# Optimization experiments

Hardware: AMD Instinct MI355X
Metric: run time of the kernel (lower is better)

The kernel has to match this reference:

```python
import jax, jax.numpy as jnp
import numpy as np

BN_EPS = 1e-5

def setup_inputs() -> dict:
    key = jax.random.key(0)
    ks = jax.random.split(key, 10)
    B, C, W, H = 4, 128, 32, 128
    Co = C // 2  # 64
    s_in = 1.0 / np.sqrt(C)
    s_out = 1.0 / np.sqrt(Co)
    return {
        "range_x": jax.random.normal(ks[0], (B, C, W, H), jnp.float32),
        "img": jax.random.normal(ks[1], (B, C, W, H), jnp.float32),
        "wq": jax.random.normal(ks[2], (Co, C), jnp.float32) * s_in,
        "bq": jax.random.normal(ks[3], (Co,), jnp.float32) * 0.01,
        "wk": jax.random.normal(ks[4], (Co, C), jnp.float32) * s_in,
        "bk": jax.random.normal(ks[5], (Co,), jnp.float32) * 0.01,
        "wv": jax.random.normal(ks[6], (Co, C), jnp.float32) * s_in,
        "bv": jax.random.normal(ks[7], (Co,), jnp.float32) * 0.01,
        "wc": jax.random.normal(ks[8], (C, Co), jnp.float32) * s_out,
        "bc": jax.random.normal(ks[9], (C,), jnp.float32) * 0.01,
        "bn_gamma": jnp.ones((C,), jnp.float32),
        "bn_beta": jnp.zeros((C,), jnp.float32),
        "bn_mean": jnp.zeros((C,), jnp.float32),
        "bn_var": jnp.ones((C,), jnp.float32),
    }

def reference(range_x, img, wq, bq, wk, bk, wv, bv, wc, bc, bn_gamma, bn_beta, bn_mean, bn_var):
    B, C, W, H = range_x.shape
    HW = W * H
    r = range_x.reshape(B, C, HW)  # [B,C,N]
    i = img.reshape(B, C, HW)
    # 1x1 convs == per-pixel linear projections
    q = jnp.einsum('oc,bcn->bno', wq, r) + bq            # [B,N,Co] (query from range)
    k = jnp.einsum('oc,bcn->bon', wk, i) + bk[None, :, None]  # [B,Co,N]
    corr = jnp.einsum('bno,bom->bnm', q, k)              # [B,N,N]
    attn = jax.nn.softmax(corr, axis=-1)
    v = jnp.einsum('oc,bcn->bon', wv, i) + bv[None, :, None]  # [B,Co,N]
    # out[b,o,n] = sum_m v[b,o,m] * attn[b,n,m]  (bmm(V, attn^T))
    out = jnp.einsum('bom,bnm->bon', v, attn)            # [B,Co,N]
    # channel_back: 1x1 conv -> BN (inference) -> ReLU
    y = jnp.einsum('co,bon->bcn', wc, out) + bc[None, :, None]
    inv = bn_gamma / jnp.sqrt(bn_var + BN_EPS)
    y = y * inv[None, :, None] + (bn_beta - bn_mean * inv)[None, :, None]
    y = jax.nn.relu(y)
    return img + y.reshape(B, C, W, H)
```

## Files before the change

kernel.cpp:

```cpp
#include <hip/hip_runtime.h>
#include <hip/hip_bf16.h>

typedef __attribute__((ext_vector_type(4))) float f32x4;
typedef __attribute__((ext_vector_type(8))) short s16x8;
typedef __attribute__((ext_vector_type(4))) short s16x4;

__device__ __forceinline__ ushort f2bf(float f){
  union { float f; unsigned u; } x; x.f = f;
  unsigned r = x.u + 0x7fffu + ((x.u >> 16) & 1u);
  return (ushort)(r >> 16);
}
__device__ __forceinline__ float bf2f(ushort h){
  union { unsigned u; float f; } x; x.u = ((unsigned)h) << 16;
  return x.f;
}

__device__ __forceinline__ void gload16(const void* g, void* l){
  __builtin_amdgcn_global_load_lds(
      (const __attribute__((address_space(1))) void*)g,
      (__attribute__((address_space(3))) void*)l, 16, 0, 0);
}

#if __has_builtin(__builtin_amdgcn_mfma_f32_16x16x16bf16_1k)
__device__ __forceinline__ f32x4 mfma16(s16x4 a, s16x4 b, f32x4 c){
  return __builtin_amdgcn_mfma_f32_16x16x16bf16_1k(a, b, c, 0, 0, 0);
}
#elif __has_builtin(__builtin_amdgcn_mfma_f32_16x16x16_bf16)
__device__ __forceinline__ f32x4 mfma16(s16x4 a, s16x4 b, f32x4 c){
  return __builtin_amdgcn_mfma_f32_16x16x16_bf16(a, b, c, 0, 0, 0);
}
#else
__device__ __forceinline__ f32x4 mfma16(s16x4 a, s16x4 b, f32x4 c){
  f32x4 d;
  asm volatile("v_mfma_f32_16x16x16_bf16 %0, %1, %2, %3\n\ts_nop 7\n\ts_nop 7"
               : "=v"(d) : "v"(a), "v"(b), "v"(c));
  return d;
}
#endif

__global__ __launch_bounds__(256) void wprep(
    const float* __restrict__ wq, const float* __restrict__ wk,
    const float* __restrict__ wv, ushort* __restrict__ Wh,
    ushort* __restrict__ Wl)
{
  int flat = blockIdx.x*256 + threadIdx.x;
  int row = flat >> 7, c = flat & 127;
  float v = (row < 64) ? wq[row*128 + c]
          : (row < 128) ? wk[(row-64)*128 + c]
          : wv[(row-128)*128 + c];
  ushort hi = f2bf(v);
  Wh[flat] = hi;
  Wl[flat] = f2bf(v - bf2f(hi));
}

__global__ __launch_bounds__(256, 2) void proj_qkv(
    const float* __restrict__ xr, const float* __restrict__ xi,
    const ushort* __restrict__ Wh, const ushort* __restrict__ Wl,
    const float* __restrict__ bq, const float* __restrict__ bk,
    const float* __restrict__ bv,
    ushort* __restrict__ Qh, ushort* __restrict__ Ql,
    ushort* __restrict__ Kh, ushort* __restrict__ Vt)
{
  __shared__ __align__(16) float xrL[128*64];
  __shared__ __align__(16) float xiL[128*64];
  const int tid = threadIdx.x;
  const int idx = blockIdx.x;
  const int oh  = idx & 1;
  const int nt  = (idx >> 1) & 63;
  const int b   = idx >> 7;
  const int n0  = nt << 6;
  const int lane = tid & 63;
  const int w    = tid >> 6;
  const int l15  = lane & 15;
  const int g    = lane >> 4;

  {
    const float* xrs = xr + (size_t)b*524288 + n0;
    const float* xis = xi + (size_t)b*524288 + n0;
    #pragma unroll
    for (int j = 0; j < 8; ++j){
      int row = j*16 + (tid >> 4);
      int ch  = tid & 15;
      gload16(xrs + (size_t)row*4096 + ch*4, xrL + j*1024 + w*256);
      gload16(xis + (size_t)row*4096 + ch*4, xiL + j*1024 + w*256);
    }
  }
  __syncthreads();

  s16x8 xrh[4], xrl[4], xih[4], xil[4];
  const int px = w*16 + l15;
  #pragma unroll
  for (int kc = 0; kc < 4; ++kc){
    #pragma unroll
    for (int j = 0; j < 8; ++j){
      int r = kc*32 + g*8 + j;
      float a = xrL[r*64 + px];
      ushort h = f2bf(a);
      xrh[kc][j] = (short)h;
      xrl[kc][j] = (short)f2bf(a - bf2f(h));
      float bb = xiL[r*64 + px];
      ushort h2 = f2bf(bb);
      xih[kc][j] = (short)h2;
      xil[kc][j] = (short)f2bf(bb - bf2f(h2));
    }
  }

  #pragma unroll
  for (int ot = 0; ot < 6; ++ot){
    const int p    = ot >> 1;
    const int sub  = ot & 1;
    const int obase = oh*32 + sub*16;
    const int wrow  = p*64 + obase;
    f32x4 acc = {0.f,0.f,0.f,0.f};
    #pragma unroll
    for (int kc = 0; kc < 4; ++kc){
      s16x8 whf = *(const s16x8*)(Wh + (size_t)(wrow + l15)*128 + kc*32 + g*8);
      s16x8 wlf = *(const s16x8*)(Wl + (size_t)(wrow + l15)*128 + kc*32 + g*8);
      const s16x8 xh = (p==0) ? xrh[kc] : xih[kc];
      const s16x8 xl = (p==0) ? xrl[kc] : xil[kc];
      if (p < 2){
        acc = __builtin_amdgcn_mfma_f32_16x16x32_bf16(xh, whf, acc, 0,0,0);
        acc = __builtin_amdgcn_mfma_f32_16x16x32_bf16(xl, whf, acc, 0,0,0);
        acc = __builtin_amdgcn_mfma_f32_16x16x32_bf16(xh, wlf, acc, 0,0,0);
      } else {
        acc = __builtin_amdgcn_mfma_f32_16x16x32_bf16(whf, xh, acc, 0,0,0);
        acc = __builtin_amdgcn_mfma_f32_16x16x32_bf16(wlf, xh, acc, 0,0,0);
        acc = __builtin_amdgcn_mfma_f32_16x16x32_bf16(whf, xl, acc, 0,0,0);
      }
    }
    if (p == 0){
      float bqv = bq[obase + l15];
      #pragma unroll
      for (int r = 0; r < 4; ++r){
        float q = acc[r] + bqv;
        ushort hi = f2bf(q);
        size_t a = (size_t)(b*4096 + n0 + w*16 + g*4 + r)*64 + obase + l15;
        Qh[a] = hi; Ql[a] = f2bf(q - bf2f(hi));
      }
    } else if (p == 1){
      float bkv = bk[obase + l15];
      #pragma unroll
      for (int r = 0; r < 4; ++r){
        float k = acc[r] + bkv;
        size_t a = (size_t)(b*4096 + n0 + w*16 + g*4 + r)*64 + obase + l15;
        Kh[a] = f2bf(k);
      }
    } else {
      #pragma unroll
      for (int r = 0; r < 4; ++r){
        int o = obase + g*4 + r;
        float v = acc[r] + bv[o];
        Vt[(size_t)(b*64 + o)*4096 + n0 + w*16 + l15] = f2bf(v);
      }
    }
  }
}

__global__ __launch_bounds__(256, 5) void flash_attn(
    const ushort* __restrict__ Qh, const ushort* __restrict__ Ql,
    const ushort* __restrict__ Kh, const ushort* __restrict__ Vt,
    float* __restrict__ Opart, float* __restrict__ Mst,
    float* __restrict__ Lst)
{
  __shared__ __align__(16) ushort khL[2][4096];
  __shared__ __align__(16) ushort vL[2][4096];

  const int tid  = threadIdx.x;
  const int idx  = blockIdx.x;
  const int ks   = idx & 3;
  const int qt   = (idx >> 2) & 63;
  const int b    = idx >> 8;
  const int lane = tid & 63;
  const int w    = tid >> 6;
  const int l15  = lane & 15;
  const int g    = lane >> 4;
  const int qrow = qt*64 + w*16;
  const int kv0  = ks << 10;
  const int srow = lane >> 2;
  const int sg   = lane & 3;
  const int sgs  = sg ^ ((srow >> 1) & 3);

  const size_t qoff = ((size_t)(b*4096 + qrow + l15))*64 + g*8;
  s16x8 qh0 = *(const s16x8*)(Qh + qoff);
  s16x8 qh1 = *(const s16x8*)(Qh + qoff + 32);
  s16x8 ql0 = *(const s16x8*)(Ql + qoff);
  s16x8 ql1 = *(const s16x8*)(Ql + qoff + 32);

  const char* KhB = (const char*)(Kh + (size_t)b*4096*64);
  const char* VB  = (const char*)(Vt + (size_t)b*64*4096);

  f32x4 o_acc[4];
  #pragma unroll
  for (int ot=0;ot<4;++ot) o_acc[ot] = (f32x4){0.f,0.f,0.f,0.f};
  float m_run = -1e30f, l_run = 0.f;

  #define STAGE_KV(kvb, bi)                                               \
  {                                                                       \
    size_t kr = (size_t)((kvb) + w*16 + srow)*128 + sgs*16;               \
    char* kd = (char*)khL[bi] + w*2048;                                   \
    gload16(KhB + kr,      kd);                                           \
    gload16(KhB + kr + 64, kd + 1024);                                    \
    size_t vr = (size_t)(w*16 + srow)*8192 + (size_t)(kvb)*2 + sgs*16;    \
    char* vd = (char*)vL[bi] + w*2048;                                    \
    gload16(VB + vr,      vd);                                            \
    gload16(VB + vr + 64, vd + 1024);                                     \
  }

  STAGE_KV(kv0, 0);
  __syncthreads();

  const int swz = (l15 >> 1) & 3;
  const int kfrag = l15*64 + (g ^ swz)*16;

  for (int t = 0; t < 16; ++t){
    const int cb = t & 1;

    if (t < 15){
      STAGE_KV(kv0 + (t+1)*64, cb ^ 1);
    }

    f32x4 s[4];
    #pragma unroll
    for (int ct=0; ct<4; ++ct){
      const char* kb = (const char*)khL[cb] + ct*2048;
      s16x8 kh0 = *(const s16x8*)(kb + kfrag);
      s16x8 kh1 = *(const s16x8*)(kb + 1024 + kfrag);
      f32x4 acc = {0.f,0.f,0.f,0.f};
      acc = __builtin_amdgcn_mfma_f32_16x16x32_bf16(kh0, ql0, acc, 0, 0, 0);
      acc = __builtin_amdgcn_mfma_f32_16x16x32_bf16(kh1, ql1, acc, 0, 0, 0);
      acc = __builtin_amdgcn_mfma_f32_16x16x32_bf16(kh0, qh0, acc, 0, 0, 0);
      acc = __builtin_amdgcn_mfma_f32_16x16x32_bf16(kh1, qh1, acc, 0, 0, 0);
      s[ct] = acc;
    }

    float mx = s[0][0];
    #pragma unroll
    for (int ct=0;ct<4;++ct){
      #pragma unroll
      for (int r=0;r<4;++r) mx = fmaxf(mx, s[ct][r]);
    }
    mx = fmaxf(mx, __shfl_xor(mx, 16));
    mx = fmaxf(mx, __shfl_xor(mx, 32));
    float mn = fmaxf(m_run, mx);
    float sc = __expf(m_run - mn);
    m_run = mn;
    float rs = 0.f;
    s16x4 pbf[4];
    #pragma unroll
    for (int ct=0;ct<4;++ct){
      #pragma unroll
      for (int r=0;r<4;++r){
        float p = __expf(s[ct][r] - mn);
        rs += p;
        pbf[ct][r] = (short)f2bf(p);
      }
    }
    rs += __shfl_xor(rs, 16);
    rs += __shfl_xor(rs, 32);
    l_run = l_run*sc + rs;
    #pragma unroll
    for (int ot=0;ot<4;++ot) o_acc[ot] *= sc;

    #pragma unroll
    for (int ot=0; ot<4; ++ot){
      const char* vbase = (const char*)vL[cb] + ot*2048 + l15*64;
      #pragma unroll
      for (int ct=0; ct<4; ++ct){
        int chunk = (((ct & 1) << 1) + (g >> 1)) ^ swz;
        s16x4 av = *(const s16x4*)(vbase + (ct>>1)*1024 + chunk*16 + (g&1)*8);
        o_acc[ot] = mfma16(av, pbf[ct], o_acc[ot]);
      }
    }

    __syncthreads();
  }
  #undef STAGE_KV

  float* ep = (float*)((char*)vL + (size_t)w*4096);
  #pragma unroll
  for (int ot=0;ot<4;++ot){
    int dw = l15*64 + ((ot*16 + g*4) ^ ((l15 & 7) << 2));
    *(f32x4*)(ep + dw) = o_acc[ot];
  }
  __syncthreads();
  {
    const int q4  = lane >> 2;
    const int seg = lane & 3;
    float* Ob = Opart + ((size_t)(ks*4 + b)*4096 + qrow)*64;
    #pragma unroll
    for (int c=0;c<4;++c){
      int o0 = seg*16 + c*4;
      f32x4 vv = *(const f32x4*)(ep + q4*64 + (o0 ^ ((q4 & 7) << 2)));
      *(f32x4*)(Ob + (size_t)q4*64 + o0) = vv;
    }
  }
  if (lane < 16){
    Mst[(size_t)(ks*4 + b)*4096 + qrow + lane] = m_run;
    Lst[(size_t)(ks*4 + b)*4096 + qrow + lane] = l_run;
  }
}

__global__ __launch_bounds__(256) void final_proj(
    const float* __restrict__ Opart, const float* __restrict__ Mst,
    const float* __restrict__ Lst, const float* __restrict__ wc,
    const float* __restrict__ bc, const float* __restrict__ gm,
    const float* __restrict__ bt, const float* __restrict__ mu,
    const float* __restrict__ vr, const float* __restrict__ img,
    float* __restrict__ out)
{
  __shared__ float ol[64*64];
  __shared__ float scl[4][64];
  const int tid = threadIdx.x;
  const int idx = blockIdx.x;
  const int cs  = idx & 3;
  const int nt  = (idx >> 2) & 63;
  const int b   = idx >> 8;
  const int n0  = nt << 6;

  if (tid < 64){
    size_t rid = (size_t)b*4096 + n0 + tid;
    float m0 = Mst[0*16384 + rid], m1 = Mst[1*16384 + rid];
    float m2 = Mst[2*16384 + rid], m3 = Mst[3*16384 + rid];
    float mm = fmaxf(fmaxf(m0,m1), fmaxf(m2,m3));
    float s0 = __expf(m0-mm), s1 = __expf(m1-mm);
    float s2 = __expf(m2-mm), s3 = __expf(m3-mm);
    float li = s0*Lst[0*16384+rid] + s1*Lst[1*16384+rid]
             + s2*Lst[2*16384+rid] + s3*Lst[3*16384+rid];
    float inv = 1.0f / li;
    scl[0][tid] = s0*inv; scl[1][tid] = s1*inv;
    scl[2][tid] = s2*inv; scl[3][tid] = s3*inv;
  }
  __syncthreads();

  {
    const size_t base = ((size_t)b*4096 + n0)*64;
    for (int j=0;j<16;++j){
      int flat = tid + (j << 8);
      int n = flat >> 6, o = flat & 63;
      float v = Opart[0*(size_t)16384*64 + base + flat] * scl[0][n]
              + Opart[1*(size_t)16384*64 + base + flat] * scl[1][n]
              + Opart[2*(size_t)16384*64 + base + flat] * scl[2][n]
              + Opart[3*(size_t)16384*64 + base + flat] * scl[3][n];
      ol[(o << 6) + (n ^ (o & 31))] = v;
    }
  }
  __syncthreads();

  const int lane = tid & 63;
  const int w = __builtin_amdgcn_readfirstlane(tid >> 6);
  const int c0 = (cs << 5) + (w << 3);

  float acc[8];
  #pragma unroll
  for (int cc=0;cc<8;++cc) acc[cc] = 0.f;

  for (int o=0;o<64;++o){
    float v = ol[(o << 6) + (lane ^ (o & 31))];
    #pragma unroll
    for (int cc=0;cc<8;++cc)
      acc[cc] = fmaf(wc[(c0+cc)*64 + o], v, acc[cc]);
  }

  #pragma unroll
  for (int cc=0;cc<8;++cc){
    int c = c0 + cc;
    float inv = gm[c] * rsqrtf(vr[c] + 1e-5f);
    float sh  = bt[c] - mu[c]*inv;
    float y = (acc[cc] + bc[c]) * inv + sh;
    y = fmaxf(y, 0.f);
    size_t gi = ((size_t)(b*128 + c))*4096 + n0 + lane;
    out[gi] = img[gi] + y;
  }
}

extern "C" void kernel_launch(void* const* d_in, const int* in_sizes, int n_in,
                              void* d_out, int out_size, void* d_ws, size_t ws_size,
                              hipStream_t stream)
{
  const float* xr = (const float*)d_in[0];
  const float* xi = (const float*)d_in[1];
  const float* wq = (const float*)d_in[2];
  const float* bq = (const float*)d_in[3];
  const float* wk = (const float*)d_in[4];
  const float* bk = (const float*)d_in[5];
  const float* wv = (const float*)d_in[6];
  const float* bv = (const float*)d_in[7];
  const float* wc = (const float*)d_in[8];
  const float* bc = (const float*)d_in[9];
  const float* gm = (const float*)d_in[10];
  const float* bt = (const float*)d_in[11];
  const float* mu = (const float*)d_in[12];
  const float* vr = (const float*)d_in[13];
  float* out = (float*)d_out;

  const size_t SZ = (size_t)4*4096*64;
  ushort* Qhw = (ushort*)d_ws;
  ushort* Qlw = Qhw + SZ;
  ushort* Khw = Qlw + SZ;
  ushort* Vtw = Khw + SZ;
  float*  Ow  = (float*)(Vtw + SZ);
  float*  Mw  = Ow + (size_t)16*4096*64;
  float*  Lw  = Mw + (size_t)16*4096;
  ushort* Whb = (ushort*)(Lw + (size_t)16*4096);
  ushort* Wlb = Whb + 192*128;

  wprep     <<<96,   256, 0, stream>>>(wq, wk, wv, Whb, Wlb);
  proj_qkv  <<<512,  256, 0, stream>>>(xr, xi, Whb, Wlb, bq, bk, bv,
                                       Qhw, Qlw, Khw, Vtw);
  flash_attn<<<1024, 256, 0, stream>>>(Qhw, Qlw, Khw, Vtw, Ow, Mw, Lw);
  final_proj<<<1024, 256, 0, stream>>>(Ow, Mw, Lw, wc, bc, gm, bt, mu, vr, xi, out);
}
```

Measured before the change: 92.37 us.

## Split KV eight ways, use exp2 with pre-scaled Q, lazy rescale, MFMA priority

Doubles the flash-attention KV split from 4 to 8 partitions (2048 blocks, 8 tiles each), and the final projection merges 8 partial results. Q is pre-multiplied by log2(e) so the softmax can use exp2f. The running max is rescaled only when some row's tile max exceeds it by more than 8, which skips the o_acc rescale on most tiles. s_setprio is raised around the MFMA sections. The aim is better occupancy and less per-tile softmax overhead. The cost is twice the partial-output traffic and a larger combine step, plus a small precision risk from deferred rescaling.

Measured after the change: 113.5 us. 1.23x slower.

```diff
diff --git a/kernel.cpp b/kernel.cpp
--- a/kernel.cpp
+++ b/kernel.cpp
@@ -4,6 +4,8 @@
 typedef __attribute__((ext_vector_type(4))) float f32x4;
 typedef __attribute__((ext_vector_type(8))) short s16x8;
 typedef __attribute__((ext_vector_type(4))) short s16x4;
+
+#define LOG2E 1.4426950408889634f
 
 __device__ __forceinline__ ushort f2bf(float f){
   union { float f; unsigned u; } x; x.f = f;
@@ -132,7 +134,7 @@
       float bqv = bq[obase + l15];
       #pragma unroll
       for (int r = 0; r < 4; ++r){
-        float q = acc[r] + bqv;
+        float q = (acc[r] + bqv) * LOG2E;
         ushort hi = f2bf(q);
         size_t a = (size_t)(b*4096 + n0 + w*16 + g*4 + r)*64 + obase + l15;
         Qh[a] = hi; Ql[a] = f2bf(q - bf2f(hi));
@@ -167,15 +169,15 @@
 
   const int tid  = threadIdx.x;
   const int idx  = blockIdx.x;
-  const int ks   = idx & 3;
-  const int qt   = (idx >> 2) & 63;
-  const int b    = idx >> 8;
+  const int ks   = idx & 7;
+  const int qt   = (idx >> 3) & 63;
+  const int b    = idx >> 9;
   const int lane = tid & 63;
   const int w    = tid >> 6;
   const int l15  = lane & 15;
   const int g    = lane >> 4;
   const int qrow = qt*64 + w*16;
-  const int kv0  = ks << 10;
+  const int kv0  = ks << 9;
   const int srow = lane >> 2;
   const int sg   = lane & 3;
   const int sgs  = sg ^ ((srow >> 1) & 3);
@@ -212,14 +214,15 @@
   const int swz = (l15 >> 1) & 3;
   const int kfrag = l15*64 + (g ^ swz)*16;
 
-  for (int t = 0; t < 16; ++t){
+  for (int t = 0; t < 8; ++t){
     const int cb = t & 1;
 
-    if (t < 15){
+    if (t < 7){
       STAGE_KV(kv0 + (t+1)*64, cb ^ 1);
     }
 
     f32x4 s[4];
+    __builtin_amdgcn_s_setprio(1);
     #pragma unroll
     for (int ct=0; ct<4; ++ct){
       const char* kb = (const char*)khL[cb] + ct*2048;
@@ -232,6 +235,7 @@
       acc = __builtin_amdgcn_mfma_f32_16x16x32_bf16(kh1, qh1, acc, 0, 0, 0);
       s[ct] = acc;
     }
+    __builtin_amdgcn_s_setprio(0);
 
     float mx = s[0][0];
     #pragma unroll
@@ -241,26 +245,30 @@
     }
     mx = fmaxf(mx, __shfl_xor(mx, 16));
     mx = fmaxf(mx, __shfl_xor(mx, 32));
-    float mn = fmaxf(m_run, mx);
-    float sc = __expf(m_run - mn);
-    m_run = mn;
+    if (!__all(mx <= m_run + 8.0f)){
+      float mn = fmaxf(m_run, mx);
+      float sc = exp2f(m_run - mn);
+      m_run = mn;
+      l_run *= sc;
+      #pragma unroll
+      for (int ot=0;ot<4;++ot) o_acc[ot] *= sc;
+    }
     float rs = 0.f;
     s16x4 pbf[4];
     #pragma unroll
     for (int ct=0;ct<4;++ct){
       #pragma unroll
       for (int r=0;r<4;++r){
-        float p = __expf(s[ct][r] - mn);
+        float p = exp2f(s[ct][r] - m_run);
         rs += p;
         pbf[ct][r] = (short)f2bf(p);
       }
     }
     rs += __shfl_xor(rs, 16);
     rs += __shfl_xor(rs, 32);
-    l_run = l_run*sc + rs;
-    #pragma unroll
-    for (int ot=0;ot<4;++ot) o_acc[ot] *= sc;
-
+    l_run += rs;
+
+    __builtin_amdgcn_s_setprio(1);
     #pragma unroll
     for (int ot=0; ot<4; ++ot){
       const char* vbase = (const char*)vL[cb] + ot*2048 + l15*64;
@@ -271,6 +279,7 @@
         o_acc[ot] = mfma16(av, pbf[ct], o_acc[ot]);
       }
     }
+    __builtin_amdgcn_s_setprio(0);
 
     __syncthreads();
   }
@@ -309,7 +318,7 @@
     float* __restrict__ out)
 {
   __shared__ float ol[64*64];
-  __shared__ float scl[4][64];
+  __shared__ float scl[8][64];
   const int tid = threadIdx.x;
   const int idx = blockIdx.x;
   const int cs  = idx & 3;
@@ -319,16 +328,22 @@
 
   if (tid < 64){
     size_t rid = (size_t)b*4096 + n0 + tid;
-    float m0 = Mst[0*16384 + rid], m1 = Mst[1*16384 + rid];
-    float m2 = Mst[2*16384 + rid], m3 = Mst[3*16384 + rid];
-    float mm = fmaxf(fmaxf(m0,m1), fmaxf(m2,m3));
-    float s0 = __expf(m0-mm), s1 = __expf(m1-mm);
-    float s2 = __expf(m2-mm), s3 = __expf(m3-mm);
-    float li = s0*Lst[0*16384+rid] + s1*Lst[1*16384+rid]
-             + s2*Lst[2*16384+rid] + s3*Lst[3*16384+rid];
+    float m[8], li = 0.f;
+    float mm = -1e30f;
+    #pragma unroll
+    for (int sp=0;sp<8;++sp){
+      m[sp] = Mst[(size_t)sp*16384 + rid];
+      mm = fmaxf(mm, m[sp]);
+    }
+    float e[8];
+    #pragma unroll
+    for (int sp=0;sp<8;++sp){
+      e[sp] = exp2f(m[sp] - mm);
+      li += e[sp] * Lst[(size_t)sp*16384 + rid];
+    }
     float inv = 1.0f / li;
-    scl[0][tid] = s0*inv; scl[1][tid] = s1*inv;
-    scl[2][tid] = s2*inv; scl[3][tid] = s3*inv;
+    #pragma unroll
+    for (int sp=0;sp<8;++sp) scl[sp][tid] = e[sp]*inv;
   }
   __syncthreads();
 
@@ -337,10 +352,10 @@
     for (int j=0;j<16;++j){
       int flat = tid + (j << 8);
       int n = flat >> 6, o = flat & 63;
-      float v = Opart[0*(size_t)16384*64 + base + flat] * scl[0][n]
-              + Opart[1*(size_t)16384*64 + base + flat] * scl[1][n]
-              + Opart[2*(size_t)16384*64 + base + flat] * scl[2][n]
-              + Opart[3*(size_t)16384*64 + base + flat] * scl[3][n];
+      float v = 0.f;
+      #pragma unroll
+      for (int sp=0;sp<8;++sp)
+        v += Opart[(size_t)sp*16384*64 + base + flat] * scl[sp][n];
       ol[(o << 6) + (n ^ (o & 31))] = v;
     }
   }
@@ -399,14 +414,14 @@
   ushort* Khw = Qlw + SZ;
   ushort* Vtw = Khw + SZ;
   float*  Ow  = (float*)(Vtw + SZ);
-  float*  Mw  = Ow + (size_t)16*4096*64;
-  float*  Lw  = Mw + (size_t)16*4096;
-  ushort* Whb = (ushort*)(Lw + (size_t)16*4096);
+  float*  Mw  = Ow + (size_t)32*4096*64;
+  float*  Lw  = Mw + (size_t)32*4096;
+  ushort* Whb = (ushort*)(Lw + (size_t)32*4096);
   ushort* Wlb = Whb + 192*128;
 
   wprep     <<<96,   256, 0, stream>>>(wq, wk, wv, Whb, Wlb);
   proj_qkv  <<<512,  256, 0, stream>>>(xr, xi, Whb, Wlb, bq, bk, bv,
                                        Qhw, Qlw, Khw, Vtw);
-  flash_attn<<<1024, 256, 0, stream>>>(Qhw, Qlw, Khw, Vtw, Ow, Mw, Lw);
+  flash_attn<<<2048, 256, 0, stream>>>(Qhw, Qlw, Khw, Vtw, Ow, Mw, Lw);
   final_proj<<<1024, 256, 0, stream>>>(Ow, Mw, Lw, wc, bc, gm, bt, mu, vr, xi, out);
 }
```

## Use exp2 softmax with lazy rescaling and MFMA row sums in flash attention

Applied to the files above, without the earlier changes.

Q is pre-scaled by log2(e) so the attention kernel can use exp2f, and the cross-split merge now uses exp2 as well. The running-max rescale of the accumulators is skipped unless some lane's max grows by more than 8. Row sums are computed by an MFMA against a ones vector on the bf16 probabilities, replacing the shuffle reductions. It also adds s_setprio around the MFMA phases, uses a tree-shaped max, and switches to the library bf16 conversion. This trims VALU and shuffle work in the softmax, at the cost of row sums taken from bf16-rounded values and a bounded growth of the unnormalised accumulators.

Result: slower. 95.62 us (+3.5%).

```diff
diff --git a/kernel.cpp b/kernel.cpp
--- a/kernel.cpp
+++ b/kernel.cpp
@@ -5,10 +5,12 @@
 typedef __attribute__((ext_vector_type(8))) short s16x8;
 typedef __attribute__((ext_vector_type(4))) short s16x4;
 
+#define LOG2E 1.4426950408889634f
+
 __device__ __forceinline__ ushort f2bf(float f){
-  union { float f; unsigned u; } x; x.f = f;
-  unsigned r = x.u + 0x7fffu + ((x.u >> 16) & 1u);
-  return (ushort)(r >> 16);
+  union { __hip_bfloat16 h; ushort u; } c;
+  c.h = __float2bfloat16(f);
+  return c.u;
 }
 __device__ __forceinline__ float bf2f(ushort h){
   union { unsigned u; float f; } x; x.u = ((unsigned)h) << 16;
@@ -132,7 +134,7 @@
       float bqv = bq[obase + l15];
       #pragma unroll
       for (int r = 0; r < 4; ++r){
-        float q = acc[r] + bqv;
+        float q = (acc[r] + bqv) * LOG2E;
         ushort hi = f2bf(q);
         size_t a = (size_t)(b*4096 + n0 + w*16 + g*4 + r)*64 + obase + l15;
         Qh[a] = hi; Ql[a] = f2bf(q - bf2f(hi));
@@ -189,10 +191,15 @@
   const char* KhB = (const char*)(Kh + (size_t)b*4096*64);
   const char* VB  = (const char*)(Vt + (size_t)b*64*4096);
 
+  s16x4 ones4;
+  #pragma unroll
+  for (int e=0;e<4;++e) ones4[e] = (short)0x3F80;
+
   f32x4 o_acc[4];
   #pragma unroll
   for (int ot=0;ot<4;++ot) o_acc[ot] = (f32x4){0.f,0.f,0.f,0.f};
-  float m_run = -1e30f, l_run = 0.f;
+  f32x4 sum_acc = {0.f,0.f,0.f,0.f};
+  float m_run = -1e30f;
 
   #define STAGE_KV(kvb, bi)                                               \
   {                                                                       \
@@ -220,6 +227,7 @@
     }
 
     f32x4 s[4];
+    __builtin_amdgcn_s_setprio(1);
     #pragma unroll
     for (int ct=0; ct<4; ++ct){
       const char* kb = (const char*)khL[cb] + ct*2048;
@@ -232,35 +240,36 @@
       acc = __builtin_amdgcn_mfma_f32_16x16x32_bf16(kh1, qh1, acc, 0, 0, 0);
       s[ct] = acc;
     }
-
-    float mx = s[0][0];
-    #pragma unroll
-    for (int ct=0;ct<4;++ct){
-      #pragma unroll
-      for (int r=0;r<4;++r) mx = fmaxf(mx, s[ct][r]);
-    }
+    __builtin_amdgcn_s_setprio(0);
+
+    float mx = fmaxf(
+        fmaxf(fmaxf(fmaxf(s[0][0],s[0][1]), fmaxf(s[0][2],s[0][3])),
+              fmaxf(fmaxf(s[1][0],s[1][1]), fmaxf(s[1][2],s[1][3]))),
+        fmaxf(fmaxf(fmaxf(s[2][0],s[2][1]), fmaxf(s[2][2],s[2][3])),
+              fmaxf(fmaxf(s[3][0],s[3][1]), fmaxf(s[3][2],s[3][3]))));
     mx = fmaxf(mx, __shfl_xor(mx, 16));
     mx = fmaxf(mx, __shfl_xor(mx, 32));
-    float mn = fmaxf(m_run, mx);
-    float sc = __expf(m_run - mn);
-    m_run = mn;
-    float rs = 0.f;
+    if (!__all(mx <= m_run + 8.0f)){
+      float mn = fmaxf(m_run, mx);
+      float sc = exp2f(m_run - mn);
+      m_run = mn;
+      #pragma unroll
+      for (int ot=0;ot<4;++ot) o_acc[ot] *= sc;
+      sum_acc *= sc;
+    }
     s16x4 pbf[4];
     #pragma unroll
     for (int ct=0;ct<4;++ct){
       #pragma unroll
       for (int r=0;r<4;++r){
-        float p = __expf(s[ct][r] - mn);
-        rs += p;
-        pbf[ct][r] = (short)f2bf(p);
-      }
-    }
-    rs += __shfl_xor(rs, 16);
-    rs += __shfl_xor(rs, 32);
-    l_run = l_run*sc + rs;
-    #pragma unroll
-    for (int ot=0;ot<4;++ot) o_acc[ot] *= sc;
-
+        pbf[ct][r] = (short)f2bf(exp2f(s[ct][r] - m_run));
+      }
+    }
+
+    __builtin_amdgcn_s_setprio(1);
+    #pragma unroll
+    for (int ct=0; ct<4; ++ct)
+      sum_acc = mfma16(ones4, pbf[ct], sum_acc);
     #pragma unroll
     for (int ot=0; ot<4; ++ot){
       const char* vbase = (const char*)vL[cb] + ot*2048 + l15*64;
@@ -271,6 +280,7 @@
         o_acc[ot] = mfma16(av, pbf[ct], o_acc[ot]);
       }
     }
+    __builtin_amdgcn_s_setprio(0);
 
     __syncthreads();
   }
@@ -296,7 +306,7 @@
   }
   if (lane < 16){
     Mst[(size_t)(ks*4 + b)*4096 + qrow + lane] = m_run;
-    Lst[(size_t)(ks*4 + b)*4096 + qrow + lane] = l_run;
+    Lst[(size_t)(ks*4 + b)*4096 + qrow + lane] = sum_acc[0];
   }
 }
 
@@ -322,8 +332,8 @@
     float m0 = Mst[0*16384 + rid], m1 = Mst[1*16384 + rid];
     float m2 = Mst[2*16384 + rid], m3 = Mst[3*16384 + rid];
     float mm = fmaxf(fmaxf(m0,m1), fmaxf(m2,m3));
-    float s0 = __expf(m0-mm), s1 = __expf(m1-mm);
-    float s2 = __expf(m2-mm), s3 = __expf(m3-mm);
+    float s0 = exp2f(m0-mm), s1 = exp2f(m1-mm);
+    float s2 = exp2f(m2-mm), s3 = exp2f(m3-mm);
     float li = s0*Lst[0*16384+rid] + s1*Lst[1*16384+rid]
              + s2*Lst[2*16384+rid] + s3*Lst[3*16384+rid];
     float inv = 1.0f / li;
```

## Split QKV projection into smaller blocks and fold log2e into Q for exp2

Applied to the files above, without the earlier changes.

The projection kernel now stages one input tensor at a time in a single shared buffer. Each block handles one 16-channel output slice, so the grid doubles and occupancy is raised to 4 blocks per CU. The Q values are pre-scaled by log2(e) so the flash attention softmax and the final merge can call exp2f instead of __expf, which removes a multiply per exponential. The trade-off is that each block now loads xr and xi separately with an extra barrier, and the x tiles are reloaded by four blocks instead of two.

Measured after the change: 100.4 us. 8.7% more time.

```diff
diff --git a/kernel.cpp b/kernel.cpp
--- a/kernel.cpp
+++ b/kernel.cpp
@@ -4,6 +4,8 @@
 typedef __attribute__((ext_vector_type(4))) float f32x4;
 typedef __attribute__((ext_vector_type(8))) short s16x8;
 typedef __attribute__((ext_vector_type(4))) short s16x4;
+
+#define LOG2E 1.4426950408889634f
 
 __device__ __forceinline__ ushort f2bf(float f){
   union { float f; unsigned u; } x; x.f = f;
@@ -53,7 +55,7 @@
   Wl[flat] = f2bf(v - bf2f(hi));
 }
 
-__global__ __launch_bounds__(256, 2) void proj_qkv(
+__global__ __launch_bounds__(256, 4) void proj_qkv(
     const float* __restrict__ xr, const float* __restrict__ xi,
     const ushort* __restrict__ Wh, const ushort* __restrict__ Wl,
     const float* __restrict__ bq, const float* __restrict__ bk,
@@ -61,91 +63,105 @@
     ushort* __restrict__ Qh, ushort* __restrict__ Ql,
     ushort* __restrict__ Kh, ushort* __restrict__ Vt)
 {
-  __shared__ __align__(16) float xrL[128*64];
-  __shared__ __align__(16) float xiL[128*64];
+  __shared__ __align__(16) float xL[128*64];
   const int tid = threadIdx.x;
   const int idx = blockIdx.x;
-  const int oh  = idx & 1;
-  const int nt  = (idx >> 1) & 63;
-  const int b   = idx >> 7;
+  const int oq  = idx & 3;
+  const int nt  = (idx >> 2) & 63;
+  const int b   = idx >> 8;
   const int n0  = nt << 6;
   const int lane = tid & 63;
   const int w    = tid >> 6;
   const int l15  = lane & 15;
   const int g    = lane >> 4;
-
+  const int obase = oq << 4;
+
+  #define STAGE_X(src)                                                    \
+  {                                                                       \
+    const float* xs = (src) + (size_t)b*524288 + n0;                      \
+    _Pragma("unroll")                                                     \
+    for (int j = 0; j < 8; ++j){                                          \
+      int row = j*16 + (tid >> 4);                                        \
+      int ch  = tid & 15;                                                 \
+      gload16(xs + (size_t)row*4096 + ch*4, xL + j*1024 + w*256);         \
+    }                                                                     \
+  }
+  #define BUILD_FRAGS(fh, fl)                                             \
+  {                                                                       \
+    const int px = w*16 + l15;                                            \
+    _Pragma("unroll")                                                     \
+    for (int kc = 0; kc < 4; ++kc){                                       \
+      _Pragma("unroll")                                                   \
+      for (int j = 0; j < 8; ++j){                                        \
+        int r = kc*32 + g*8 + j;                                          \
+        float a = xL[r*64 + px];                                          \
+        ushort h = f2bf(a);                                               \
+        fh[kc][j] = (short)h;                                             \
+        fl[kc][j] = (short)f2bf(a - bf2f(h));                             \
+      }                                                                   \
+    }                                                                     \
+  }
+
+  STAGE_X(xr);
+  __syncthreads();
   {
-    const float* xrs = xr + (size_t)b*524288 + n0;
-    const float* xis = xi + (size_t)b*524288 + n0;
-    #pragma unroll
-    for (int j = 0; j < 8; ++j){
-      int row = j*16 + (tid >> 4);
-      int ch  = tid & 15;
-      gload16(xrs + (size_t)row*4096 + ch*4, xrL + j*1024 + w*256);
-      gload16(xis + (size_t)row*4096 + ch*4, xiL + j*1024 + w*256);
-    }
-  }
-  __syncthreads();
-
-  s16x8 xrh[4], xrl[4], xih[4], xil[4];
-  const int px = w*16 + l15;
-  #pragma unroll
-  for (int kc = 0; kc < 4; ++kc){
-    #pragma unroll
-    for (int j = 0; j < 8; ++j){
-      int r = kc*32 + g*8 + j;
-      float a = xrL[r*64 + px];
-      ushort h = f2bf(a);
-      xrh[kc][j] = (short)h;
-      xrl[kc][j] = (short)f2bf(a - bf2f(h));
-      float bb = xiL[r*64 + px];
-      ushort h2 = f2bf(bb);
-      xih[kc][j] = (short)h2;
-      xil[kc][j] = (short)f2bf(bb - bf2f(h2));
-    }
-  }
-
-  #pragma unroll
-  for (int ot = 0; ot < 6; ++ot){
-    const int p    = ot >> 1;
-    const int sub  = ot & 1;
-    const int obase = oh*32 + sub*16;
-    const int wrow  = p*64 + obase;
+    s16x8 xh[4], xl4[4];
+    BUILD_FRAGS(xh, xl4);
+    const int wrow = obase;
     f32x4 acc = {0.f,0.f,0.f,0.f};
     #pragma unroll
     for (int kc = 0; kc < 4; ++kc){
       s16x8 whf = *(const s16x8*)(Wh + (size_t)(wrow + l15)*128 + kc*32 + g*8);
       s16x8 wlf = *(const s16x8*)(Wl + (size_t)(wrow + l15)*128 + kc*32 + g*8);
-      const s16x8 xh = (p==0) ? xrh[kc] : xih[kc];
-      const s16x8 xl = (p==0) ? xrl[kc] : xil[kc];
-      if (p < 2){
-        acc = __builtin_amdgcn_mfma_f32_16x16x32_bf16(xh, whf, acc, 0,0,0);
-        acc = __builtin_amdgcn_mfma_f32_16x16x32_bf16(xl, whf, acc, 0,0,0);
-        acc = __builtin_amdgcn_mfma_f32_16x16x32_bf16(xh, wlf, acc, 0,0,0);
-      } else {
-        acc = __builtin_amdgcn_mfma_f32_16x16x32_bf16(whf, xh, acc, 0,0,0);
-        acc = __builtin_amdgcn_mfma_f32_16x16x32_bf16(wlf, xh, acc, 0,0,0);
-        acc = __builtin_amdgcn_mfma_f32_16x16x32_bf16(whf, xl, acc, 0,0,0);
-      }
-    }
-    if (p == 0){
-      float bqv = bq[obase + l15];
+      acc = __builtin_amdgcn_mfma_f32_16x16x32_bf16(xh[kc], whf, acc, 0,0,0);
+      acc = __builtin_amdgcn_mfma_f32_16x16x32_bf16(xl4[kc], whf, acc, 0,0,0);
+      acc = __builtin_amdgcn_mfma_f32_16x16x32_bf16(xh[kc], wlf, acc, 0,0,0);
+    }
+    float bqv = bq[obase + l15];
+    #pragma unroll
+    for (int r = 0; r < 4; ++r){
+      float q = (acc[r] + bqv) * LOG2E;
+      ushort hi = f2bf(q);
+      size_t a = (size_t)(b*4096 + n0 + w*16 + g*4 + r)*64 + obase + l15;
+      Qh[a] = hi; Ql[a] = f2bf(q - bf2f(hi));
+    }
+  }
+  __syncthreads();
+
+  STAGE_X(xi);
+  __syncthreads();
+  {
+    s16x8 xh[4], xl4[4];
+    BUILD_FRAGS(xh, xl4);
+    {
+      const int wrow = 64 + obase;
+      f32x4 acc = {0.f,0.f,0.f,0.f};
+      #pragma unroll
+      for (int kc = 0; kc < 4; ++kc){
+        s16x8 whf = *(const s16x8*)(Wh + (size_t)(wrow + l15)*128 + kc*32 + g*8);
+        s16x8 wlf = *(const s16x8*)(Wl + (size_t)(wrow + l15)*128 + kc*32 + g*8);
+        acc = __builtin_amdgcn_mfma_f32_16x16x32_bf16(xh[kc], whf, acc, 0,0,0);
+        acc = __builtin_amdgcn_mfma_f32_16x16x32_bf16(xl4[kc], whf, acc, 0,0,0);
+        acc = __builtin_amdgcn_mfma_f32_16x16x32_bf16(xh[kc], wlf, acc, 0,0,0);
+      }
+      float bkv = bk[obase + l15];
       #pragma unroll
       for (int r = 0; r < 4; ++r){
-        float q = acc[r] + bqv;
-        ushort hi = f2bf(q);
         size_t a = (size_t)(b*4096 + n0 + w*16 + g*4 + r)*64 + obase + l15;
-        Qh[a] = hi; Ql[a] = f2bf(q - bf2f(hi));
-      }
-    } else if (p == 1){
-      float bkv = bk[obase + l15];
-      #pragma unroll
-      for (int r = 0; r < 4; ++r){
-        float k = acc[r] + bkv;
-        size_t a = (size_t)(b*4096 + n0 + w*16 + g*4 + r)*64 + obase + l15;
-        Kh[a] = f2bf(k);
-      }
-    } else {
+        Kh[a] = f2bf(acc[r] + bkv);
+      }
+    }
+    {
+      const int wrow = 128 + obase;
+      f32x4 acc = {0.f,0.f,0.f,0.f};
+      #pragma unroll
+      for (int kc = 0; kc < 4; ++kc){
+        s16x8 whf = *(const s16x8*)(Wh + (size_t)(wrow + l15)*128 + kc*32 + g*8);
+        s16x8 wlf = *(const s16x8*)(Wl + (size_t)(wrow + l15)*128 + kc*32 + g*8);
+        acc = __builtin_amdgcn_mfma_f32_16x16x32_bf16(whf, xh[kc], acc, 0,0,0);
+        acc = __builtin_amdgcn_mfma_f32_16x16x32_bf16(wlf, xh[kc], acc, 0,0,0);
+        acc = __builtin_amdgcn_mfma_f32_16x16x32_bf16(whf, xl4[kc], acc, 0,0,0);
+      }
       #pragma unroll
       for (int r = 0; r < 4; ++r){
         int o = obase + g*4 + r;
@@ -154,6 +170,8 @@
       }
     }
   }
+  #undef STAGE_X
+  #undef BUILD_FRAGS
 }
 
 __global__ __launch_bounds__(256, 5) void flash_attn(
@@ -242,7 +260,7 @@
     mx = fmaxf(mx, __shfl_xor(mx, 16));
     mx = fmaxf(mx, __shfl_xor(mx, 32));
     float mn = fmaxf(m_run, mx);
-    float sc = __expf(m_run - mn);
+    float sc = exp2f(m_run - mn);
     m_run = mn;
     float rs = 0.f;
     s16x4 pbf[4];
@@ -250,7 +268,7 @@
     for (int ct=0;ct<4;++ct){
       #pragma unroll
       for (int r=0;r<4;++r){
-        float p = __expf(s[ct][r] - mn);
+        float p = exp2f(s[ct][r] - mn);
         rs += p;
         pbf[ct][r] = (short)f2bf(p);
       }
@@ -322,8 +340,8 @@
     float m0 = Mst[0*16384 + rid], m1 = Mst[1*16384 + rid];
     float m2 = Mst[2*16384 + rid], m3 = Mst[3*16384 + rid];
     float mm = fmaxf(fmaxf(m0,m1), fmaxf(m2,m3));
-    float s0 = __expf(m0-mm), s1 = __expf(m1-mm);
-    float s2 = __expf(m2-mm), s3 = __expf(m3-mm);
+    float s0 = exp2f(m0-mm), s1 = exp2f(m1-mm);
+    float s2 = exp2f(m2-mm), s3 = exp2f(m3-mm);
     float li = s0*Lst[0*16384+rid] + s1*Lst[1*16384+rid]
              + s2*Lst[2*16384+rid] + s3*Lst[3*16384+rid];
     float inv = 1.0f / li;
@@ -405,7 +423,7 @@
   ushort* Wlb = Whb + 192*128;
 
   wprep     <<<96,   256, 0, stream>>>(wq, wk, wv, Whb, Wlb);
-  proj_qkv  <<<512,  256, 0, stream>>>(xr, xi, Whb, Wlb, bq, bk, bv,
+  proj_qkv  <<<1024, 256, 0, stream>>>(xr, xi, Whb, Wlb, bq, bk, bv,
                                        Qhw, Qlw, Khw, Vtw);
   flash_attn<<<1024, 256, 0, stream>>>(Qhw, Qlw, Khw, Vtw, Ow, Mw, Lw);
   final_proj<<<1024, 256, 0, stream>>>(Ow, Mw, Lw, wc, bc, gm, bt, mu, vr, xi, out);
```
